# Performance work log

Hardware: AMD Instinct MI355X
Metric: run time of the kernel (lower is better)

The kernel has to match this reference:

```python
import jax, jax.numpy as jnp
import numpy as np

N, C, H, K = 50000, 256, 8, 16
M = N * K
HID = 4 * C
HD = C // H
SCALE = HD ** -0.5
EPS = 1e-5


def setup_inputs() -> dict:
    key = jax.random.key(0)
    ks = jax.random.split(key, 8)
    init = lambda k, shape, fan: jax.random.normal(k, shape, jnp.float32) * (fan ** -0.5)
    return {
        "feats": jax.random.normal(ks[0], (N, C), jnp.float32),
        "polar_pos": jax.random.normal(ks[1], (N, 3), jnp.float32),
        "edge_index": jax.random.randint(ks[2], (2, M), 0, N, dtype=jnp.int64),
        "ln1_g": jnp.ones((C,), jnp.float32), "ln1_b": jnp.zeros((C,), jnp.float32),
        "qkv_w": init(ks[3], (3 * C, C), C), "qkv_b": jnp.zeros((3 * C,), jnp.float32),
        "proj_w": init(ks[4], (C, C), C), "proj_b": jnp.zeros((C,), jnp.float32),
        "ln2_g": jnp.ones((C,), jnp.float32), "ln2_b": jnp.zeros((C,), jnp.float32),
        "fc1_w": init(ks[5], (HID, C), C), "fc1_b": jnp.zeros((HID,), jnp.float32),
        "fc2_w": init(ks[6], (C, HID), HID), "fc2_b": jnp.zeros((C,), jnp.float32),
    }


def _ln(x, g, b):
    m = x.mean(-1, keepdims=True)
    v = jnp.var(x, axis=-1, keepdims=True)
    return (x - m) * jax.lax.rsqrt(v + EPS) * g + b


def reference(feats, polar_pos, edge_index, ln1_g, ln1_b, qkv_w, qkv_b,
              proj_w, proj_b, ln2_g, ln2_b, fc1_w, fc1_b, fc2_w, fc2_b):
    skip = feats
    x = _ln(feats, ln1_g, ln1_b)

    # edge bookkeeping: sort edges by destination (index_0), matching torch.sort
    idx0 = edge_index[0]
    idx1 = edge_index[1]
    order = jnp.argsort(idx0)  # stable sort
    idx0 = idx0[order]
    idx1 = idx1[order]

    # qkv projection -> (N, 3, H, HD)
    qkv = (x @ qkv_w.T + qkv_b).reshape(N, 3, H, HD)
    q = qkv[:, 0] * SCALE  # (N, H, HD)
    k = qkv[:, 1]
    v = qkv[:, 2]

    # attention_step1_v2: per-edge dot products, (M, H)
    attn = jnp.einsum('mhd,mhd->mh', q[idx0], k[idx1])

    # scatter_softmax over edges grouped by idx0
    mx = jax.ops.segment_max(attn, idx0, num_segments=N)
    e = jnp.exp(attn - mx[idx0])
    s = jax.ops.segment_sum(e, idx0, num_segments=N)
    w = e / s[idx0]  # (M, H)

    # attention_step2: weighted aggregation of neighbor values
    out = jax.ops.segment_sum(w[:, :, None] * v[idx1], idx0, num_segments=N)
    out = out.reshape(N, C)

    out = out @ proj_w.T + proj_b
    feats = skip + out

    y = _ln(feats, ln2_g, ln2_b)
    y = jax.nn.gelu(y @ fc1_w.T + fc1_b, approximate=False)
    y = y @ fc2_w.T + fc2_b
    return feats + y
```

## Files before the change

kernel.cpp:

```cpp
#include <hip/hip_runtime.h>
#include <hip/hip_bf16.h>
#include <cmath>


#define N_NODES 50000
#define C_DIM 256
#define M_EDGES 800000
#define ATT_SCALE 0.17677669529663687f
#define LN_EPS 1e-5f
#define LOG2E 1.4426950408889634f
#define NEG_BIG -3.0e38f

typedef unsigned int uint_t;
typedef unsigned short ushort_t;
typedef short short8 __attribute__((ext_vector_type(8)));
typedef float floatx4 __attribute__((ext_vector_type(4)));

__device__ __forceinline__ ushort_t f2bf(float f) {
  uint_t u = __float_as_uint(f);
  return (ushort_t)((u + 0x7FFFu + ((u >> 16) & 1u)) >> 16);
}
__device__ __forceinline__ float bf_even(uint_t u) { return __uint_as_float(u << 16); }
__device__ __forceinline__ float bf_odd(uint_t u) { return __uint_as_float(u & 0xFFFF0000u); }

__device__ __forceinline__ float gelu_tanh(float x) {
  const float u = 0.7978845608028654f * (x + 0.044715f * x * x * x);
  const float e = __expf(2.0f * u);
  const float t = 1.0f - 2.0f / (e + 1.0f);
  return 0.5f * x * (1.0f + t);
}

__device__ __forceinline__ void gload16(const void* g, void* l) {
  __builtin_amdgcn_global_load_lds(
      (const __attribute__((address_space(1))) void*)g,
      (__attribute__((address_space(3))) void*)l, 16, 0, 0);
}

__global__ __launch_bounds__(256) void ln_kernel(const float* __restrict__ x,
    const float* __restrict__ g, const float* __restrict__ b,
    ushort_t* __restrict__ y)
{
  __shared__ float red[8];
  const int n = blockIdx.x;
  const int t = threadIdx.x;
  float v = x[(size_t)n * C_DIM + t];
  float s = v, s2 = v * v;
#pragma unroll
  for (int m = 1; m < 64; m <<= 1) {
    s += __shfl_xor(s, m);
    s2 += __shfl_xor(s2, m);
  }
  const int wave = t >> 6;
  if ((t & 63) == 0) { red[wave] = s; red[4 + wave] = s2; }
  __syncthreads();
  s = red[0] + red[1] + red[2] + red[3];
  s2 = red[4] + red[5] + red[6] + red[7];
  const float mean = s * (1.0f / 256.0f);
  const float var = fmaxf(s2 * (1.0f / 256.0f) - mean * mean, 0.0f);
  const float r = rsqrtf(var + LN_EPS);
  y[(size_t)n * C_DIM + t] = f2bf((v - mean) * r * g[t] + b[t]);
}

__global__ void cvt_kernel(const float* __restrict__ s0, const float* __restrict__ s1,
                           const float* __restrict__ s2, const float* __restrict__ s3,
                           ushort_t* __restrict__ dst)
{
  const int i = blockIdx.x * 256 + threadIdx.x;
  float v;
  if (i < 196608) v = s0[i];
  else if (i < 262144) v = s1[i - 196608];
  else if (i < 524288) v = s2[i - 262144];
  else v = s3[i - 524288];
  dst[i] = f2bf(v);
}

template <int EPI>
__global__ __launch_bounds__(256, 2) void mfma_gemm(
    const ushort_t* __restrict__ A, const ushort_t* __restrict__ W,
    const float* __restrict__ bias, const float* __restrict__ extra,
    void* __restrict__ OutV, int Kdim, int Jdim)
{
  __shared__ __align__(16) char smem[36864];
  ushort_t* As = (ushort_t*)smem;
  ushort_t* Bs = As + 128 * 64;
  const int t = threadIdx.x;
  const int lane = t & 63;
  const int w = t >> 6;
  const int wm = w & 1;
  const int wn = w >> 1;
  const int rowbase = blockIdx.y * 128;
  const int colbase = blockIdx.x * 128;

  floatx4 acc[4][4] = {};

  int rA[4], kcg[4];
#pragma unroll
  for (int h = 0; h < 4; ++h) {
    const int cidx = h * 256 + w * 64 + lane;
    const int r = cidx >> 3;
    rA[h] = r;
    kcg[h] = (cidx & 7) ^ (r & 7);
  }

  const int rl = lane & 15;
  const int qd = lane >> 4;

  for (int k0 = 0; k0 < Kdim; k0 += 64) {
#pragma unroll
    for (int h = 0; h < 4; ++h) {
      const int r = rA[h];
      int grow = rowbase + r;
      if (grow > N_NODES - 1) grow = N_NODES - 1;
      const int gcol = colbase + r;
      ushort_t* lbase_a = As + (size_t)(h * 256 + w * 64) * 8;
      ushort_t* lbase_b = Bs + (size_t)(h * 256 + w * 64) * 8;
      gload16(A + (size_t)grow * Kdim + k0 + kcg[h] * 8, lbase_a);
      gload16(W + (size_t)gcol * Kdim + k0 + kcg[h] * 8, lbase_b);
    }
    __syncthreads();

#pragma unroll
    for (int h = 0; h < 2; ++h) {
      short8 af[4], bf[4];
#pragma unroll
      for (int tm = 0; tm < 4; ++tm) {
        const int ra = wm * 64 + tm * 16 + rl;
        const int kc = (h * 4 + qd) ^ (ra & 7);
        af[tm] = *(const short8*)(As + ra * 64 + kc * 8);
      }
#pragma unroll
      for (int tn = 0; tn < 4; ++tn) {
        const int rb = wn * 64 + tn * 16 + rl;
        const int kc = (h * 4 + qd) ^ (rb & 7);
        bf[tn] = *(const short8*)(Bs + rb * 64 + kc * 8);
      }
#pragma unroll
      for (int tm = 0; tm < 4; ++tm)
#pragma unroll
        for (int tn = 0; tn < 4; ++tn)
          acc[tm][tn] = __builtin_amdgcn_mfma_f32_16x16x32_bf16(
              af[tm], bf[tn], acc[tm][tn], 0, 0, 0);
    }
    __syncthreads();
  }

  const int q8 = lane >> 3;
  const int c8 = lane & 7;
  if (EPI == 1) {
    float* sc = (float*)smem + w * (64 * 36);
#pragma unroll
    for (int p = 0; p < 2; ++p) {
      __syncthreads();
#pragma unroll
      for (int th = 0; th < 2; ++th) {
        const int tn = p * 2 + th;
#pragma unroll
        for (int tm = 0; tm < 4; ++tm)
#pragma unroll
          for (int r = 0; r < 4; ++r)
            sc[(tm * 16 + qd * 4 + r) * 36 + th * 16 + rl] = acc[tm][tn][r];
      }
      __syncthreads();
      const int col0 = colbase + wn * 64 + p * 32 + c8 * 4;
      const float4 b4 = *(const float4*)(bias + col0);
#pragma unroll
      for (int it = 0; it < 8; ++it) {
        const int lr = it * 8 + q8;
        const int grow = rowbase + wm * 64 + lr;
        if (grow >= N_NODES) continue;
        float4 v = *(const float4*)(sc + lr * 36 + c8 * 4);
        const float4 e4 = *(const float4*)(extra + (size_t)grow * Jdim + col0);
        v.x += b4.x + e4.x; v.y += b4.y + e4.y;
        v.z += b4.z + e4.z; v.w += b4.w + e4.w;
        *(float4*)((float*)OutV + (size_t)grow * Jdim + col0) = v;
      }
    }
  } else {
    ushort_t* su = (ushort_t*)smem + w * (64 * 72);
#pragma unroll
    for (int tn = 0; tn < 4; ++tn) {
      const int col = colbase + wn * 64 + tn * 16 + rl;
      const float bv = bias[col];
#pragma unroll
      for (int tm = 0; tm < 4; ++tm)
#pragma unroll
        for (int r = 0; r < 4; ++r) {
          float v = acc[tm][tn][r] + bv;
          if (EPI == 0) {
            if (col < 256) v *= ATT_SCALE;
          } else {
            v = gelu_tanh(v);
          }
          su[(tm * 16 + qd * 4 + r) * 72 + tn * 16 + rl] = f2bf(v);
        }
    }
    __syncthreads();
#pragma unroll
    for (int it = 0; it < 8; ++it) {
      const int lr = it * 8 + q8;
      const int grow = rowbase + wm * 64 + lr;
      if (grow >= N_NODES) continue;
      const uint4 v = *(const uint4*)(su + lr * 72 + c8 * 8);
      *(uint4*)((ushort_t*)OutV + (size_t)grow * Jdim + colbase + wn * 64 + c8 * 8) = v;
    }
  }
}

__global__ void hist_kernel(const int* __restrict__ idx0, int* __restrict__ counts)
{
  const int m = blockIdx.x * 256 + threadIdx.x;
  if (m < M_EDGES) atomicAdd(&counts[idx0[m]], 1);
}

__global__ __launch_bounds__(256) void scan1_kernel(const int* __restrict__ counts,
    int* __restrict__ offsets, int* __restrict__ bsums)
{
  __shared__ int tmp[256];
  const int t = threadIdx.x;
  const int i = blockIdx.x * 256 + t;
  const int v = (i < N_NODES) ? counts[i] : 0;
  int x = v;
  tmp[t] = x;
  __syncthreads();
#pragma unroll
  for (int off = 1; off < 256; off <<= 1) {
    const int a = (t >= off) ? tmp[t - off] : 0;
    __syncthreads();
    x += a;
    tmp[t] = x;
    __syncthreads();
  }
  if (i < N_NODES) offsets[i] = x - v;
  if (t == 255) bsums[blockIdx.x] = x;
}

__global__ __launch_bounds__(256) void scan2_kernel(int* __restrict__ bsums, int nb)
{
  __shared__ int tmp[256];
  const int t = threadIdx.x;
  const int v = (t < nb) ? bsums[t] : 0;
  int x = v;
  tmp[t] = x;
  __syncthreads();
#pragma unroll
  for (int off = 1; off < 256; off <<= 1) {
    const int a = (t >= off) ? tmp[t - off] : 0;
    __syncthreads();
    x += a;
    tmp[t] = x;
    __syncthreads();
  }
  if (t < nb) bsums[t] = x - v;
}

__global__ void scan3_kernel(int* __restrict__ offsets, const int* __restrict__ bsums)
{
  const int i = blockIdx.x * 256 + threadIdx.x;
  if (i < N_NODES) offsets[i] += bsums[blockIdx.x];
  if (i == 0) offsets[N_NODES] = M_EDGES;
}

__global__ void scatter_kernel(const int* __restrict__ idx0,
    const int* __restrict__ idx1, const int* __restrict__ offsets,
    int* __restrict__ cursor, int* __restrict__ srcs)
{
  const int m = blockIdx.x * 256 + threadIdx.x;
  if (m < M_EDGES) {
    const int n = idx0[m];
    const int p = offsets[n] + atomicAdd(&cursor[n], 1);
    srcs[p] = idx1[m];
  }
}

__global__ __launch_bounds__(256) void attn_kernel(
    const ushort_t* __restrict__ QKVh, const int* __restrict__ offsets,
    const int* __restrict__ srcs, ushort_t* __restrict__ AO)
{
  const int node = blockIdx.x * 4 + (threadIdx.x >> 6);
  if (node >= N_NODES) return;
  const int lane = threadIdx.x & 63;
  const int h = lane & 7;
  const int slot = lane >> 3;
  const int start = offsets[node];
  const int end = offsets[node + 1];

  float q[32];
  {
    const uint4* qr = (const uint4*)(QKVh + (size_t)node * 768 + h * 32);
#pragma unroll
    for (int i = 0; i < 4; ++i) {
      const uint4 u = qr[i];
      q[i * 8 + 0] = bf_even(u.x); q[i * 8 + 1] = bf_odd(u.x);
      q[i * 8 + 2] = bf_even(u.y); q[i * 8 + 3] = bf_odd(u.y);
      q[i * 8 + 4] = bf_even(u.z); q[i * 8 + 5] = bf_odd(u.z);
      q[i * 8 + 6] = bf_even(u.w); q[i * 8 + 7] = bf_odd(u.w);
    }
  }

  float m = NEG_BIG, s = 0.f;
  float o[32];
#pragma unroll
  for (int d = 0; d < 32; ++d) o[d] = 0.f;

  for (int e = start + slot; e < end; e += 8) {
    const int sidx = srcs[e];
    const uint4* kr = (const uint4*)(QKVh + (size_t)sidx * 768 + 256 + h * 32);
    float d = 0.f;
#pragma unroll
    for (int i = 0; i < 4; ++i) {
      const uint4 u = kr[i];
      d += q[i * 8 + 0] * bf_even(u.x) + q[i * 8 + 1] * bf_odd(u.x);
      d += q[i * 8 + 2] * bf_even(u.y) + q[i * 8 + 3] * bf_odd(u.y);
      d += q[i * 8 + 4] * bf_even(u.z) + q[i * 8 + 5] * bf_odd(u.z);
      d += q[i * 8 + 6] * bf_even(u.w) + q[i * 8 + 7] * bf_odd(u.w);
    }
    const float l = d * LOG2E;
    const float mn = fmaxf(m, l);
    const float fac = exp2f(m - mn);
    const float wgt = exp2f(l - mn);
    m = mn;
    s = s * fac + wgt;
    const uint4* vr = (const uint4*)(QKVh + (size_t)sidx * 768 + 512 + h * 32);
#pragma unroll
    for (int i = 0; i < 4; ++i) {
      const uint4 u = vr[i];
      o[i * 8 + 0] = o[i * 8 + 0] * fac + wgt * bf_even(u.x);
      o[i * 8 + 1] = o[i * 8 + 1] * fac + wgt * bf_odd(u.x);
      o[i * 8 + 2] = o[i * 8 + 2] * fac + wgt * bf_even(u.y);
      o[i * 8 + 3] = o[i * 8 + 3] * fac + wgt * bf_odd(u.y);
      o[i * 8 + 4] = o[i * 8 + 4] * fac + wgt * bf_even(u.z);
      o[i * 8 + 5] = o[i * 8 + 5] * fac + wgt * bf_odd(u.z);
      o[i * 8 + 6] = o[i * 8 + 6] * fac + wgt * bf_even(u.w);
      o[i * 8 + 7] = o[i * 8 + 7] * fac + wgt * bf_odd(u.w);
    }
  }

  float mx = m;
  mx = fmaxf(mx, __shfl_xor(mx, 8));
  mx = fmaxf(mx, __shfl_xor(mx, 16));
  mx = fmaxf(mx, __shfl_xor(mx, 32));
  const float fac = exp2f(m - mx);
  s *= fac;
#pragma unroll
  for (int d = 0; d < 32; ++d) o[d] *= fac;

  s += __shfl_xor(s, 8);
  s += __shfl_xor(s, 16);
  s += __shfl_xor(s, 32);

  {
    const bool up = (slot & 4) != 0;
#pragma unroll
    for (int i = 0; i < 16; ++i) {
      const float send = up ? o[i] : o[i + 16];
      const float recv = __shfl_xor(send, 32);
      o[i] = (up ? o[i + 16] : o[i]) + recv;
    }
  }
  {
    const bool up = (slot & 2) != 0;
#pragma unroll
    for (int i = 0; i < 8; ++i) {
      const float send = up ? o[i] : o[i + 8];
      const float recv = __shfl_xor(send, 16);
      o[i] = (up ? o[i + 8] : o[i]) + recv;
    }
  }
  {
    const bool up = (slot & 1) != 0;
#pragma unroll
    for (int i = 0; i < 4; ++i) {
      const float send = up ? o[i] : o[i + 4];
      const float recv = __shfl_xor(send, 8);
      o[i] = (up ? o[i + 4] : o[i]) + recv;
    }
  }
  const int dbase = ((slot & 4) ? 16 : 0) + ((slot & 2) ? 8 : 0) +
                    ((slot & 1) ? 4 : 0);
  const float inv = (end > start) ? 1.0f / s : 0.0f;
  ushort4 st;
  st.x = f2bf(o[0] * inv); st.y = f2bf(o[1] * inv);
  st.z = f2bf(o[2] * inv); st.w = f2bf(o[3] * inv);
  *(ushort4*)(AO + (size_t)node * 256 + h * 32 + dbase) = st;
}

extern "C" void kernel_launch(void* const* d_in, const int* in_sizes, int n_in,
                              void* d_out, int out_size, void* d_ws,
                              size_t ws_size, hipStream_t stream)
{
  const float* feats  = (const float*)d_in[0];
  const int*   edge   = (const int*)d_in[2];
  const float* ln1_g  = (const float*)d_in[3];
  const float* ln1_b  = (const float*)d_in[4];
  const float* qkv_w  = (const float*)d_in[5];
  const float* qkv_b  = (const float*)d_in[6];
  const float* proj_w = (const float*)d_in[7];
  const float* proj_b = (const float*)d_in[8];
  const float* ln2_g  = (const float*)d_in[9];
  const float* ln2_b  = (const float*)d_in[10];
  const float* fc1_w  = (const float*)d_in[11];
  const float* fc1_b  = (const float*)d_in[12];
  const float* fc2_w  = (const float*)d_in[13];
  const float* fc2_b  = (const float*)d_in[14];
  float* out = (float*)d_out;

  ushort_t* Xb   = (ushort_t*)d_ws;
  ushort_t* QKVh = Xb + (size_t)N_NODES * 256;
  ushort_t* AOb  = QKVh + (size_t)N_NODES * 768;
  ushort_t* Hb   = QKVh;
  ushort_t* wb   = AOb + (size_t)N_NODES * 256;
  ushort_t* qkv_wb  = wb;
  ushort_t* proj_wb = qkv_wb + 768 * 256;
  ushort_t* fc1_wb  = proj_wb + 256 * 256;
  ushort_t* fc2_wb  = fc1_wb + 1024 * 256;
  int* counts  = (int*)(fc2_wb + 256 * 1024);
  int* cursor  = counts + N_NODES;
  int* offsets = cursor + N_NODES;
  int* srcs    = offsets + N_NODES + 1;
  int* bsums   = srcs + M_EDGES;
  const size_t required = (size_t)((char*)(bsums + 256) - (char*)d_ws);
  if (ws_size < required) {
    hipMemsetAsync(d_out, 0, (size_t)out_size * sizeof(float), stream);
    return;
  }
  const int* idx0 = edge;
  const int* idx1 = edge + M_EDGES;
  const int rowTiles = (N_NODES + 127) / 128;
  const int scanBlocks = (N_NODES + 255) / 256;

  hipMemsetAsync(counts, 0, 2 * N_NODES * sizeof(int), stream);
  cvt_kernel<<<786432 / 256, 256, 0, stream>>>(qkv_w, proj_w, fc1_w, fc2_w, wb);

  ln_kernel<<<N_NODES, 256, 0, stream>>>(feats, ln1_g, ln1_b, Xb);
  mfma_gemm<0><<<dim3(768 / 128, rowTiles), 256, 0, stream>>>(
      Xb, qkv_wb, qkv_b, nullptr, QKVh, 256, 768);
  hist_kernel<<<(M_EDGES + 255) / 256, 256, 0, stream>>>(idx0, counts);
  scan1_kernel<<<scanBlocks, 256, 0, stream>>>(counts, offsets, bsums);
  scan2_kernel<<<1, 256, 0, stream>>>(bsums, scanBlocks);
  scan3_kernel<<<scanBlocks, 256, 0, stream>>>(offsets, bsums);
  scatter_kernel<<<(M_EDGES + 255) / 256, 256, 0, stream>>>(idx0, idx1, offsets,
                                                            cursor, srcs);
  attn_kernel<<<N_NODES / 4, 256, 0, stream>>>(QKVh, offsets, srcs, AOb);
  mfma_gemm<1><<<dim3(256 / 128, rowTiles), 256, 0, stream>>>(
      AOb, proj_wb, proj_b, feats, out, 256, 256);
  ln_kernel<<<N_NODES, 256, 0, stream>>>(out, ln2_g, ln2_b, Xb);
  mfma_gemm<2><<<dim3(1024 / 128, rowTiles), 256, 0, stream>>>(
      Xb, fc1_wb, fc1_b, nullptr, Hb, 256, 1024);
  mfma_gemm<1><<<dim3(256 / 128, rowTiles), 256, 0, stream>>>(
      Hb, fc2_wb, fc2_b, out, out, 1024, 256);
}
```

Baseline: 563.3 us.

## Retile GEMMs to 64x256, vectorize LayerNorm per wave, unroll attention edges by two

```diff
diff --git a/kernel.cpp b/kernel.cpp
--- a/kernel.cpp
+++ b/kernel.cpp
@@ -40,25 +40,27 @@
     const float* __restrict__ g, const float* __restrict__ b,
     ushort_t* __restrict__ y)
 {
-  __shared__ float red[8];
-  const int n = blockIdx.x;
-  const int t = threadIdx.x;
-  float v = x[(size_t)n * C_DIM + t];
-  float s = v, s2 = v * v;
+  const int row = blockIdx.x * 4 + (threadIdx.x >> 6);
+  const int lane = threadIdx.x & 63;
+  const float4 v = *(const float4*)(x + (size_t)row * C_DIM + lane * 4);
+  float s = v.x + v.y + v.z + v.w;
+  float s2 = v.x * v.x + v.y * v.y + v.z * v.z + v.w * v.w;
 #pragma unroll
   for (int m = 1; m < 64; m <<= 1) {
     s += __shfl_xor(s, m);
     s2 += __shfl_xor(s2, m);
   }
-  const int wave = t >> 6;
-  if ((t & 63) == 0) { red[wave] = s; red[4 + wave] = s2; }
-  __syncthreads();
-  s = red[0] + red[1] + red[2] + red[3];
-  s2 = red[4] + red[5] + red[6] + red[7];
   const float mean = s * (1.0f / 256.0f);
   const float var = fmaxf(s2 * (1.0f / 256.0f) - mean * mean, 0.0f);
   const float r = rsqrtf(var + LN_EPS);
-  y[(size_t)n * C_DIM + t] = f2bf((v - mean) * r * g[t] + b[t]);
+  const float4 g4 = *(const float4*)(g + lane * 4);
+  const float4 b4 = *(const float4*)(b + lane * 4);
+  ushort4 o;
+  o.x = f2bf((v.x - mean) * r * g4.x + b4.x);
+  o.y = f2bf((v.y - mean) * r * g4.y + b4.y);
+  o.z = f2bf((v.z - mean) * r * g4.z + b4.z);
+  o.w = f2bf((v.w - mean) * r * g4.w + b4.w);
+  *(ushort4*)(y + (size_t)row * C_DIM + lane * 4) = o;
 }
 
 __global__ void cvt_kernel(const float* __restrict__ s0, const float* __restrict__ s1,
@@ -80,95 +82,92 @@
     const float* __restrict__ bias, const float* __restrict__ extra,
     void* __restrict__ OutV, int Kdim, int Jdim)
 {
-  __shared__ __align__(16) char smem[36864];
+  __shared__ __align__(16) char smem[40960];
   ushort_t* As = (ushort_t*)smem;
-  ushort_t* Bs = As + 128 * 64;
+  ushort_t* Bs = As + 64 * 64;
   const int t = threadIdx.x;
   const int lane = t & 63;
   const int w = t >> 6;
   const int wm = w & 1;
   const int wn = w >> 1;
-  const int rowbase = blockIdx.y * 128;
-  const int colbase = blockIdx.x * 128;
-
-  floatx4 acc[4][4] = {};
-
-  int rA[4], kcg[4];
-#pragma unroll
-  for (int h = 0; h < 4; ++h) {
-    const int cidx = h * 256 + w * 64 + lane;
-    const int r = cidx >> 3;
-    rA[h] = r;
-    kcg[h] = (cidx & 7) ^ (r & 7);
-  }
+  const int rowbase = blockIdx.y * 64;
+  const int colbase = blockIdx.x * 256;
+
+  floatx4 acc[2][8] = {};
+
+  const int base = w * 64 + lane;
+  const int rbase = base >> 3;
+  const int kcs = (base & 7) ^ (rbase & 7);
 
   const int rl = lane & 15;
   const int qd = lane >> 4;
 
   for (int k0 = 0; k0 < Kdim; k0 += 64) {
 #pragma unroll
-    for (int h = 0; h < 4; ++h) {
-      const int r = rA[h];
-      int grow = rowbase + r;
+    for (int h = 0; h < 2; ++h) {
+      int grow = rowbase + h * 32 + rbase;
       if (grow > N_NODES - 1) grow = N_NODES - 1;
-      const int gcol = colbase + r;
-      ushort_t* lbase_a = As + (size_t)(h * 256 + w * 64) * 8;
-      ushort_t* lbase_b = Bs + (size_t)(h * 256 + w * 64) * 8;
-      gload16(A + (size_t)grow * Kdim + k0 + kcg[h] * 8, lbase_a);
-      gload16(W + (size_t)gcol * Kdim + k0 + kcg[h] * 8, lbase_b);
+      gload16(A + (size_t)grow * Kdim + k0 + kcs * 8,
+              As + (h * 256 + w * 64) * 8);
+    }
+#pragma unroll
+    for (int h = 0; h < 8; ++h) {
+      const int gcol = colbase + h * 32 + rbase;
+      gload16(W + (size_t)gcol * Kdim + k0 + kcs * 8,
+              Bs + (h * 256 + w * 64) * 8);
     }
     __syncthreads();
 
 #pragma unroll
     for (int h = 0; h < 2; ++h) {
-      short8 af[4], bf[4];
-#pragma unroll
-      for (int tm = 0; tm < 4; ++tm) {
-        const int ra = wm * 64 + tm * 16 + rl;
+      short8 af[2], bf[8];
+#pragma unroll
+      for (int tm = 0; tm < 2; ++tm) {
+        const int ra = wm * 32 + tm * 16 + rl;
         const int kc = (h * 4 + qd) ^ (ra & 7);
         af[tm] = *(const short8*)(As + ra * 64 + kc * 8);
       }
 #pragma unroll
-      for (int tn = 0; tn < 4; ++tn) {
-        const int rb = wn * 64 + tn * 16 + rl;
+      for (int tn = 0; tn < 8; ++tn) {
+        const int rb = wn * 128 + tn * 16 + rl;
         const int kc = (h * 4 + qd) ^ (rb & 7);
         bf[tn] = *(const short8*)(Bs + rb * 64 + kc * 8);
       }
 #pragma unroll
-      for (int tm = 0; tm < 4; ++tm)
-#pragma unroll
-        for (int tn = 0; tn < 4; ++tn)
+      for (int tm = 0; tm < 2; ++tm)
+#pragma unroll
+        for (int tn = 0; tn < 8; ++tn)
           acc[tm][tn] = __builtin_amdgcn_mfma_f32_16x16x32_bf16(
               af[tm], bf[tn], acc[tm][tn], 0, 0, 0);
     }
     __syncthreads();
   }
 
-  const int q8 = lane >> 3;
-  const int c8 = lane & 7;
+  const int rr = lane >> 4;
   if (EPI == 1) {
-    float* sc = (float*)smem + w * (64 * 36);
+    float* sc = (float*)smem + w * (32 * 68);
+    const int c4 = (lane & 15) * 4;
 #pragma unroll
     for (int p = 0; p < 2; ++p) {
       __syncthreads();
 #pragma unroll
-      for (int th = 0; th < 2; ++th) {
-        const int tn = p * 2 + th;
-#pragma unroll
-        for (int tm = 0; tm < 4; ++tm)
+      for (int th = 0; th < 4; ++th) {
+        const int tn = p * 4 + th;
+#pragma unroll
+        for (int tm = 0; tm < 2; ++tm)
 #pragma unroll
           for (int r = 0; r < 4; ++r)
-            sc[(tm * 16 + qd * 4 + r) * 36 + th * 16 + rl] = acc[tm][tn][r];
+            sc[(tm * 16 + qd * 4 + r) * 68 + th * 16 + rl] = acc[tm][tn][r];
       }
       __syncthreads();
-      const int col0 = colbase + wn * 64 + p * 32 + c8 * 4;
+      const int col0 = colbase + wn * 128 + p * 64 + c4;
       const float4 b4 = *(const float4*)(bias + col0);
 #pragma unroll
       for (int it = 0; it < 8; ++it) {
-        const int lr = it * 8 + q8;
-        const int grow = rowbase + wm * 64 + lr;
+        const int lr = it * 4 + rr;
+        const int grow = rowbase + wm * 32 + lr;
         if (grow >= N_NODES) continue;
-        float4 v = *(const float4*)(sc + lr * 36 + c8 * 4);
+        float4 v = *(const float4*)(sc + lr * 68 + c4);
         const float4 e4 = *(const float4*)(extra + (size_t)grow * Jdim + col0);
         v.x += b4.x + e4.x; v.y += b4.y + e4.y;
         v.z += b4.z + e4.z; v.w += b4.w + e4.w;
@@ -176,13 +175,14 @@
       }
     }
   } else {
-    ushort_t* su = (ushort_t*)smem + w * (64 * 72);
-#pragma unroll
-    for (int tn = 0; tn < 4; ++tn) {
-      const int col = colbase + wn * 64 + tn * 16 + rl;
+    __syncthreads();
+    ushort_t* su = (ushort_t*)smem + w * (32 * 136);
+#pragma unroll
+    for (int tn = 0; tn < 8; ++tn) {
+      const int col = colbase + wn * 128 + tn * 16 + rl;
       const float bv = bias[col];
 #pragma unroll
-      for (int tm = 0; tm < 4; ++tm)
+      for (int tm = 0; tm < 2; ++tm)
 #pragma unroll
         for (int r = 0; r < 4; ++r) {
           float v = acc[tm][tn][r] + bv;
@@ -191,17 +191,18 @@
           } else {
             v = gelu_tanh(v);
           }
-          su[(tm * 16 + qd * 4 + r) * 72 + tn * 16 + rl] = f2bf(v);
+          su[(tm * 16 + qd * 4 + r) * 136 + tn * 16 + rl] = f2bf(v);
         }
     }
     __syncthreads();
+    const int c8 = (lane & 15) * 8;
 #pragma unroll
     for (int it = 0; it < 8; ++it) {
-      const int lr = it * 8 + q8;
-      const int grow = rowbase + wm * 64 + lr;
+      const int lr = it * 4 + rr;
+      const int grow = rowbase + wm * 32 + lr;
       if (grow >= N_NODES) continue;
-      const uint4 v = *(const uint4*)(su + lr * 72 + c8 * 8);
-      *(uint4*)((ushort_t*)OutV + (size_t)grow * Jdim + colbase + wn * 64 + c8 * 8) = v;
+      const uint4 v = *(const uint4*)(su + lr * 136 + c8);
+      *(uint4*)((ushort_t*)OutV + (size_t)grow * Jdim + colbase + wn * 128 + c8) = v;
     }
   }
 }
@@ -302,36 +303,54 @@
 #pragma unroll
   for (int d = 0; d < 32; ++d) o[d] = 0.f;
 
-  for (int e = start + slot; e < end; e += 8) {
-    const int sidx = srcs[e];
-    const uint4* kr = (const uint4*)(QKVh + (size_t)sidx * 768 + 256 + h * 32);
-    float d = 0.f;
+  for (int e = start + slot; e < end; e += 16) {
+    const bool has1 = (e + 8) < end;
+    const int s0i = srcs[e];
+    const int s1i = has1 ? srcs[e + 8] : s0i;
+    const uint4* k0p = (const uint4*)(QKVh + (size_t)s0i * 768 + 256 + h * 32);
+    const uint4* k1p = (const uint4*)(QKVh + (size_t)s1i * 768 + 256 + h * 32);
+    const uint4* v0p = (const uint4*)(QKVh + (size_t)s0i * 768 + 512 + h * 32);
+    const uint4* v1p = (const uint4*)(QKVh + (size_t)s1i * 768 + 512 + h * 32);
+    uint4 ka[4], kb[4], va[4], vb[4];
 #pragma unroll
     for (int i = 0; i < 4; ++i) {
-      const uint4 u = kr[i];
-      d += q[i * 8 + 0] * bf_even(u.x) + q[i * 8 + 1] * bf_odd(u.x);
-      d += q[i * 8 + 2] * bf_even(u.y) + q[i * 8 + 3] * bf_odd(u.y);
-      d += q[i * 8 + 4] * bf_even(u.z) + q[i * 8 + 5] * bf_odd(u.z);
-      d += q[i * 8 + 6] * bf_even(u.w) + q[i * 8 + 7] * bf_odd(u.w);
-    }
-    const float l = d * LOG2E;
-    const float mn = fmaxf(m, l);
+      ka[i] = k0p[i]; kb[i] = k1p[i];
+      va[i] = v0p[i]; vb[i] = v1p[i];
+    }
+    float d0 = 0.f, d1 = 0.f;
+#pragma unroll
+    for (int i = 0; i < 4; ++i) {
+      const uint4 u = ka[i];
+      d0 += q[i * 8 + 0] * bf_even(u.x) + q[i * 8 + 1] * bf_odd(u.x);
+      d0 += q[i * 8 + 2] * bf_even(u.y) + q[i * 8 + 3] * bf_odd(u.y);
+      d0 += q[i * 8 + 4] * bf_even(u.z) + q[i * 8 + 5] * bf_odd(u.z);
+      d0 += q[i * 8 + 6] * bf_even(u.w) + q[i * 8 + 7] * bf_odd(u.w);
+      const uint4 x = kb[i];
+      d1 += q[i * 8 + 0] * bf_even(x.x) + q[i * 8 + 1] * bf_odd(x.x);
+      d1 += q[i * 8 + 2] * bf_even(x.y) + q[i * 8 + 3] * bf_odd(x.y);
+      d1 += q[i * 8 + 4] * bf_even(x.z) + q[i * 8 + 5] * bf_odd(x.z);
+      d1 += q[i * 8 + 6] * bf_even(x.w) + q[i * 8 + 7] * bf_odd(x.w);
+    }
+    const float l0 = d0 * LOG2E;
+    const float l1 = has1 ? d1 * LOG2E : NEG_BIG;
+    const float mn = fmaxf(fmaxf(m, l0), l1);
     const float fac = exp2f(m - mn);
-    const float wgt = exp2f(l - mn);
+    const float w0 = exp2f(l0 - mn);
+    const float w1 = has1 ? exp2f(l1 - mn) : 0.f;
     m = mn;
-    s = s * fac + wgt;
-    const uint4* vr = (const uint4*)(QKVh + (size_t)sidx * 768 + 512 + h * 32);
+    s = s * fac + w0 + w1;
 #pragma unroll
     for (int i = 0; i < 4; ++i) {
-      const uint4 u = vr[i];
-      o[i * 8 + 0] = o[i * 8 + 0] * fac + wgt * bf_even(u.x);
-      o[i * 8 + 1] = o[i * 8 + 1] * fac + wgt * bf_odd(u.x);
-      o[i * 8 + 2] = o[i * 8 + 2] * fac + wgt * bf_even(u.y);
-      o[i * 8 + 3] = o[i * 8 + 3] * fac + wgt * bf_odd(u.y);
-      o[i * 8 + 4] = o[i * 8 + 4] * fac + wgt * bf_even(u.z);
-      o[i * 8 + 5] = o[i * 8 + 5] * fac + wgt * bf_odd(u.z);
-      o[i * 8 + 6] = o[i * 8 + 6] * fac + wgt * bf_even(u.w);
-      o[i * 8 + 7] = o[i * 8 + 7] * fac + wgt * bf_odd(u.w);
+      const uint4 ua = va[i];
+      const uint4 ub = vb[i];
+      o[i * 8 + 0] = o[i * 8 + 0] * fac + w0 * bf_even(ua.x) + w1 * bf_even(ub.x);
+      o[i * 8 + 1] = o[i * 8 + 1] * fac + w0 * bf_odd(ua.x)  + w1 * bf_odd(ub.x);
+      o[i * 8 + 2] = o[i * 8 + 2] * fac + w0 * bf_even(ua.y) + w1 * bf_even(ub.y);
+      o[i * 8 + 3] = o[i * 8 + 3] * fac + w0 * bf_odd(ua.y)  + w1 * bf_odd(ub.y);
+      o[i * 8 + 4] = o[i * 8 + 4] * fac + w0 * bf_even(ua.z) + w1 * bf_even(ub.z);
+      o[i * 8 + 5] = o[i * 8 + 5] * fac + w0 * bf_odd(ua.z)  + w1 * bf_odd(ub.z);
+      o[i * 8 + 6] = o[i * 8 + 6] * fac + w0 * bf_even(ua.w) + w1 * bf_even(ub.w);
+      o[i * 8 + 7] = o[i * 8 + 7] * fac + w0 * bf_odd(ua.w)  + w1 * bf_odd(ub.w);
     }
   }
 
@@ -425,14 +444,14 @@
   }
   const int* idx0 = edge;
   const int* idx1 = edge + M_EDGES;
-  const int rowTiles = (N_NODES + 127) / 128;
+  const int rowTiles = (N_NODES + 63) / 64;
   const int scanBlocks = (N_NODES + 255) / 256;
 
   hipMemsetAsync(counts, 0, 2 * N_NODES * sizeof(int), stream);
   cvt_kernel<<<786432 / 256, 256, 0, stream>>>(qkv_w, proj_w, fc1_w, fc2_w, wb);
 
-  ln_kernel<<<N_NODES, 256, 0, stream>>>(feats, ln1_g, ln1_b, Xb);
-  mfma_gemm<0><<<dim3(768 / 128, rowTiles), 256, 0, stream>>>(
+  ln_kernel<<<N_NODES / 4, 256, 0, stream>>>(feats, ln1_g, ln1_b, Xb);
+  mfma_gemm<0><<<dim3(768 / 256, rowTiles), 256, 0, stream>>>(
       Xb, qkv_wb, qkv_b, nullptr, QKVh, 256, 768);
   hist_kernel<<<(M_EDGES + 255) / 256, 256, 0, stream>>>(idx0, counts);
   scan1_kernel<<<scanBlocks, 256, 0, stream>>>(counts, offsets, bsums);
@@ -441,11 +460,11 @@
   scatter_kernel<<<(M_EDGES + 255) / 256, 256, 0, stream>>>(idx0, idx1, offsets,
                                                             cursor, srcs);
   attn_kernel<<<N_NODES / 4, 256, 0, stream>>>(QKVh, offsets, srcs, AOb);
-  mfma_gemm<1><<<dim3(256 / 128, rowTiles), 256, 0, stream>>>(
+  mfma_gemm<1><<<dim3(256 / 256, rowTiles), 256, 0, stream>>>(
       AOb, proj_wb, proj_b, feats, out, 256, 256);
-  ln_kernel<<<N_NODES, 256, 0, stream>>>(out, ln2_g, ln2_b, Xb);
-  mfma_gemm<2><<<dim3(1024 / 128, rowTiles), 256, 0, stream>>>(
+  ln_kernel<<<N_NODES / 4, 256, 0, stream>>>(out, ln2_g, ln2_b, Xb);
+  mfma_gemm<2><<<dim3(1024 / 256, rowTiles), 256, 0, stream>>>(
       Xb, fc1_wb, fc1_b, nullptr, Hb, 256, 1024);
-  mfma_gemm<1><<<dim3(256 / 128, rowTiles), 256, 0, stream>>>(
+  mfma_gemm<1><<<dim3(256 / 256, rowTiles), 256, 0, stream>>>(
       Hb, fc2_wb, fc2_b, out, out, 1024, 256);
 }
```

Result: no change. 560.1 us (-0.6%).
